# Performance work log

Hardware: AMD Instinct MI355X
Metric: run time of the kernel (lower is better)

Reference implementation:

```python
import jax, jax.numpy as jnp
import numpy as np


def _conv3x3(x, W, b):
    # NCHW conv, stride 1, padding 1 (hard-coded in the torch module)
    y = jax.lax.conv_general_dilated(
        x, W, window_strides=(1, 1), padding=[(1, 1), (1, 1)],
        dimension_numbers=("NCHW", "OIHW", "NCHW"))
    return y + b[None, :, None, None]


def _grid_sample_bilinear(img, gx, gy):
    # img: [N,H,W]; gx,gy: [N,H,W] normalized coords in [-1,1].
    # Matches torch grid_sample(mode='bilinear', padding_mode='zeros',
    # align_corners=False).
    N, H, W = img.shape
    ix = ((gx + 1.0) * W - 1.0) * 0.5  # unnormalized x coord
    iy = ((gy + 1.0) * H - 1.0) * 0.5  # unnormalized y coord

    x0f = jnp.floor(ix)
    y0f = jnp.floor(iy)
    x0 = x0f.astype(jnp.int32)
    y0 = y0f.astype(jnp.int32)
    x1 = x0 + 1
    y1 = y0 + 1

    # bilinear weights
    wx1 = ix - x0f
    wy1 = iy - y0f
    wx0 = 1.0 - wx1
    wy0 = 1.0 - wy1

    n_idx = jnp.arange(N)[:, None, None]

    def gather(yi, xi):
        valid = (yi >= 0) & (yi < H) & (xi >= 0) & (xi < W)
        yc = jnp.clip(yi, 0, H - 1)
        xc = jnp.clip(xi, 0, W - 1)
        v = img[n_idx, yc, xc]
        return jnp.where(valid, v, 0.0)

    return (gather(y0, x0) * (wy0 * wx0)
            + gather(y0, x1) * (wy0 * wx1)
            + gather(y1, x0) * (wy1 * wx0)
            + gather(y1, x1) * (wy1 * wx1))


def setup_inputs() -> dict:
    key = jax.random.key(0)
    ks = jax.random.split(key, 7)
    B, Cin, Cout, H, W = 16, 64, 64, 128, 128
    fan_in = Cin * 3 * 3
    std = 1.0 / np.sqrt(fan_in)
    x = jax.random.normal(ks[0], (B, Cin, H, W), dtype=jnp.float32)
    Ws = jax.random.normal(ks[1], (Cout, Cin, 3, 3), dtype=jnp.float32) * std
    Wx = jax.random.normal(ks[2], (Cout, Cin, 3, 3), dtype=jnp.float32) * std
    Wy = jax.random.normal(ks[3], (Cout, Cin, 3, 3), dtype=jnp.float32) * std
    bs = jnp.zeros((Cout,), dtype=jnp.float32)
    bx = jnp.zeros((Cout,), dtype=jnp.float32)
    by = jnp.zeros((Cout,), dtype=jnp.float32)
    return {"x": x, "Ws": Ws, "bs": bs, "Wx": Wx, "bx": bx, "Wy": Wy, "by": by}


def reference(x, Ws, bs, Wx, bx, Wy, by):
    score = _conv3x3(x, Ws, bs)            # [B,C,H,W]
    gx = _conv3x3(x, Wx, bx)               # absolute grid x coords
    gy = _conv3x3(x, Wy, by)               # absolute grid y coords
    B, C, H, W = score.shape
    out = _grid_sample_bilinear(score.reshape(B * C, H, W),
                                gx.reshape(B * C, H, W),
                                gy.reshape(B * C, H, W))
    return out.reshape(B, C, H, W)
```

## Files before the change

kernel.cpp:

```cpp
#include <hip/hip_runtime.h>
#include <stdint.h>

typedef unsigned short ushort_t;
typedef _Float16 f16x8 __attribute__((ext_vector_type(8)));
typedef _Float16 f16x4 __attribute__((ext_vector_type(4)));
typedef float f32x4 __attribute__((ext_vector_type(4)));
typedef float f32x16 __attribute__((ext_vector_type(16)));
typedef int   i32x4 __attribute__((ext_vector_type(4)));
typedef int   i32x16 __attribute__((ext_vector_type(16)));
typedef unsigned int uint4v __attribute__((ext_vector_type(4)));

#define HW_ 16384
#define MFMAH  __builtin_amdgcn_mfma_f32_32x32x16_f16
#define MFMAI8 __builtin_amdgcn_mfma_i32_32x32x32_i8
#define C_CORR (1.0f/16777216.0f)

__device__ __forceinline__ ushort_t f2h_bits(float f){
  union { _Float16 h; ushort_t u; } c; c.h = (_Float16)f; return c.u;
}
__device__ __forceinline__ float h_bits2f(ushort_t u){
  union { _Float16 h; ushort_t u; } c; c.u = u; return (float)c.h;
}
__device__ __forceinline__ int clamp8(int v){ return min(max(v,-127),127); }

__global__ __launch_bounds__(256) void k_repack(
    const float* __restrict__ Ws, const float* __restrict__ Wx,
    const float* __restrict__ Wy,
    ushort_t* __restrict__ WpH, unsigned int* __restrict__ WpC){
  int e = blockIdx.x*256 + threadIdx.x;
  if (e < 110592){
    int j = e & 7; int lane = (e >> 3) & 63; int rest = e >> 9;
    int ks = rest % 36; int cm = rest / 36;
    int conv = cm >> 1; int mh = cm & 1;
    int co = mh*32 + (lane & 31);
    int tap = ks >> 2;
    int ci = (ks & 3)*16 + ((lane >> 5) & 1)*8 + j;
    const float* src = (conv==0) ? Ws : (conv==1) ? Wx : Wy;
    WpH[e] = f2h_bits(src[(co*64 + ci)*9 + tap]);
  } else if (e < 110592 + 36864){
    int d = e - 110592;
    int j4 = d & 3; int lane = (d >> 2) & 63; int rest = d >> 8;
    int ks = rest % 18; int gm = rest / 18;
    int g = gm >> 1; int mh = gm & 1;
    int co = mh*32 + (lane & 31);
    int tap = ks >> 1;
    const float* src = (g==0 || g==2) ? Wx : Wy;
    unsigned dd = 0;
    #pragma unroll
    for (int bb=0; bb<4; bb++){
      int ci = (ks & 1)*32 + ((lane >> 5) & 1)*16 + j4*4 + bb;
      float w = src[(co*64 + ci)*9 + tap];
      int v;
      if (g < 2){
        v = clamp8((int)rintf(w*512.f));
      } else {
        float wl = w - h_bits2f(f2h_bits(w));
        v = clamp8((int)rintf(wl*1048576.f));
      }
      dd |= ((unsigned)(v & 255)) << (bb*8);
    }
    WpC[d] = dd;
  }
}

__global__ __launch_bounds__(512, 2) void k_conv_all(
    const float* __restrict__ x,
    const ushort_t* __restrict__ WpH, const unsigned int* __restrict__ WpC,
    const float* __restrict__ bs, const float* __restrict__ bx,
    const float* __restrict__ by,
    ushort_t* __restrict__ score, unsigned int* __restrict__ coords){
  int bid = blockIdx.x;
  int idx = bid >> 3;
  int b = (bid & 7) + 8*(idx >> 6);
  int rest = idx & 63;
  int h0 = (rest >> 2)*8;
  int wq = (rest & 3)*32;
  int t = threadIdx.x; int lane = t & 63; int wid = t >> 6;
  int n = lane & 31; int kh = lane >> 5;
  __shared__ __align__(16) _Float16 BH[10*34*64];
  __shared__ __align__(16) char BAl[10*34*64];
  __shared__ __align__(16) char BAh[10*34*64];

  const float* xb = x + (size_t)b*64*HW_;
  #pragma unroll
  for (int it=0; it<3; it++){
    int f = it*512 + t;
    if (f < 1360){
      int r = f/136; int rem = f - r*136; int q = rem/34; int w1 = rem - q*34;
      int y = h0 + r - 1; int w = wq + w1 - 1;
      f16x8 h0v = {0,0,0,0,0,0,0,0}, h1v = {0,0,0,0,0,0,0,0};
      unsigned alb[4] = {0,0,0,0}, ahb[4] = {0,0,0,0};
      if (((unsigned)y < 128u) & ((unsigned)w < 128u)){
        const float* p = xb + (size_t)(q*16)*HW_ + y*128 + w;
        #pragma unroll
        for (int j=0; j<16; j++){
          float v = p[(size_t)j*HW_];
          _Float16 hv = (_Float16)v;
          float al = v - (float)hv;
          int a8 = clamp8((int)rintf(al*32768.f));
          int x8 = clamp8((int)rintf(v*16.f));
          if (j < 8) h0v[j] = hv; else h1v[j-8] = hv;
          alb[j>>2] |= ((unsigned)(a8 & 255)) << ((j&3)*8);
          ahb[j>>2] |= ((unsigned)(x8 & 255)) << ((j&3)*8);
        }
      }
      int base = (r*34 + w1)*64;
      int sw = w1 & 7;
      *(f16x8*)&BH[base + (((2*q)   ^ sw) << 3)] = h0v;
      *(f16x8*)&BH[base + (((2*q+1) ^ sw) << 3)] = h1v;
      int islot = ((q + (w1 >> 1)) & 3) << 4;
      i32x4 av  = {(int)alb[0],(int)alb[1],(int)alb[2],(int)alb[3]};
      i32x4 hv2 = {(int)ahb[0],(int)ahb[1],(int)ahb[2],(int)ahb[3]};
      *(i32x4*)&BAl[base + islot] = av;
      *(i32x4*)&BAh[base + islot] = hv2;
    }
  }
  __syncthreads();

  int mh = wid & 1;
  int pp = wid >> 1;

  f32x16 acc_s0, acc_gx0, acc_gy0, acc_s1, acc_gx1, acc_gy1;
  i32x16 c_x0, c_y0, c_x1, c_y1;
  #pragma unroll
  for (int r2=0; r2<16; r2++){
    acc_s0[r2]=0.f; acc_gx0[r2]=0.f; acc_gy0[r2]=0.f;
    acc_s1[r2]=0.f; acc_gx1[r2]=0.f; acc_gy1[r2]=0.f;
    c_x0[r2]=0; c_y0[r2]=0; c_x1[r2]=0; c_y1[r2]=0;
  }

  const ushort_t* pS = WpH + ((0*2+mh)*36)*512 + lane*8;
  const ushort_t* pX = WpH + ((1*2+mh)*36)*512 + lane*8;
  const ushort_t* pY = WpH + ((2*2+mh)*36)*512 + lane*8;
  const char* pWhx = (const char*)WpC + (((0*2+mh)*18)*64 + lane)*16;
  const char* pWhy = (const char*)WpC + (((1*2+mh)*18)*64 + lane)*16;
  const char* pWlx = (const char*)WpC + (((2*2+mh)*18)*64 + lane)*16;
  const char* pWly = (const char*)WpC + (((3*2+mh)*18)*64 + lane)*16;

  #define ROWBLK(ROWB, AS_, AX_, AY_, CX_, CY_) do {                    \
    f16x8 bA  = *(const f16x8*)&BH[(ROWB) + off0];                      \
    f16x8 bB  = *(const f16x8*)&BH[(ROWB) + off1];                      \
    i32x4 bal = *(const i32x4*)&BAl[(ROWB) + islot];                    \
    i32x4 bah = *(const i32x4*)&BAh[(ROWB) + islot];                    \
    AS_ = MFMAH(sA, bA, AS_, 0,0,0);                                    \
    AX_ = MFMAH(xA, bA, AX_, 0,0,0);                                    \
    AY_ = MFMAH(yA, bA, AY_, 0,0,0);                                    \
    AS_ = MFMAH(sB, bB, AS_, 0,0,0);                                    \
    AX_ = MFMAH(xB, bB, AX_, 0,0,0);                                    \
    AY_ = MFMAH(yB, bB, AY_, 0,0,0);                                    \
    CX_ = MFMAI8(whx, bal, CX_, 0,0,0);                                 \
    CX_ = MFMAI8(wlx, bah, CX_, 0,0,0);                                 \
    CY_ = MFMAI8(why, bal, CY_, 0,0,0);                                 \
    CY_ = MFMAI8(wly, bah, CY_, 0,0,0);                                 \
  } while(0)

  #pragma unroll 1
  for (int ks=0; ks<18; ++ks){
    int tap = ks >> 1; int qp = ks & 1;
    int rb = tap/3; int dw = tap - rb*3 - 1;
    int w1 = n + dw + 1;
    int sw = w1 & 7;
    int rowb0 = ((rb + 2*pp)*34 + w1)*64;
    int rowb1 = rowb0 + 34*64;
    int off0  = ((qp*4 + kh)     ^ sw) << 3;
    int off1  = ((qp*4 + 2 + kh) ^ sw) << 3;
    int islot = (((qp*2 + kh) + (w1 >> 1)) & 3) << 4;
    f16x8 sA = *(const f16x8*)pS;
    f16x8 sB = *(const f16x8*)(pS + 512);
    f16x8 xA = *(const f16x8*)pX;
    f16x8 xB = *(const f16x8*)(pX + 512);
    f16x8 yA = *(const f16x8*)pY;
    f16x8 yB = *(const f16x8*)(pY + 512);
    i32x4 whx = *(const i32x4*)pWhx;
    i32x4 why = *(const i32x4*)pWhy;
    i32x4 wlx = *(const i32x4*)pWlx;
    i32x4 wly = *(const i32x4*)pWly;
    ROWBLK(rowb0, acc_s0, acc_gx0, acc_gy0, c_x0, c_y0);
    ROWBLK(rowb1, acc_s1, acc_gx1, acc_gy1, c_x1, c_y1);
    pS += 1024; pX += 1024; pY += 1024;
    pWhx += 1024; pWhy += 1024; pWlx += 1024; pWly += 1024;
  }
  #undef ROWBLK

  int w = wq + n;
  int hb = h0 + 2*pp;
  #define EPILOG(AS_, AX_, AY_, CX_, CY_, H_) do {                      \
    ushort_t*     sb = score  + (size_t)b*64*HW_ + (H_)*128 + w;        \
    unsigned int* cb = coords + (size_t)b*64*HW_ + (H_)*128 + w;        \
    _Pragma("unroll")                                                   \
    for (int reg=0; reg<16; reg++){                                     \
      int col = mh*32 + (reg & 3) + 8*(reg >> 2) + 4*kh;                \
      float sv = AS_[reg] + bs[col];                                    \
      float gx = AX_[reg] + (float)CX_[reg]*C_CORR + bx[col];           \
      float gy = AY_[reg] + (float)CY_[reg]*C_CORR + by[col];           \
      __builtin_nontemporal_store(f2h_bits(sv), &sb[(size_t)col*HW_]);  \
      float ixf = fminf(fmaxf((gx + 1.f)*64.f - 0.5f, -2.f), 129.f);    \
      float iyf = fminf(fmaxf((gy + 1.f)*64.f - 0.5f, -2.f), 129.f);    \
      unsigned ux = (unsigned)rintf((ixf + 4.f)*480.f);                 \
      unsigned uy = (unsigned)rintf((iyf + 4.f)*480.f);                 \
      __builtin_nontemporal_store(ux | (uy << 16), &cb[(size_t)col*HW_]); \
    }                                                                   \
  } while(0)
  EPILOG(acc_s0, acc_gx0, acc_gy0, c_x0, c_y0, hb);
  EPILOG(acc_s1, acc_gx1, acc_gy1, c_x1, c_y1, hb+1);
  #undef EPILOG
}

__global__ __launch_bounds__(256, 4) void k_sample(
    const ushort_t* __restrict__ score, const unsigned int* __restrict__ coords,
    float* __restrict__ out){
  int bid = blockIdx.x;
  int idx = bid >> 3;
  int b  = (bid & 7) + 8*(idx >> 6);
  int co = idx & 63;
  int t = threadIdx.x;
  __shared__ __align__(16) unsigned int SC32[135*68];

  #pragma unroll
  for (int i=0;i<9;i++){
    int c = i*256 + t;
    if (c < 2295){
      uint4v z = {0,0,0,0};
      *(uint4v*)&SC32[c*4] = z;
    }
  }
  __syncthreads();

  const ushort_t* sp = score + (size_t)(b*64 + co)*HW_;
  ushort_t* scu = (ushort_t*)SC32;
  #pragma unroll
  for (int i=0;i<8;i++){
    int c = i*256 + t;
    int y = c >> 4; int xg = (c & 15)*8;
    f16x8 v = __builtin_nontemporal_load((const f16x8*)(sp + c*8));
    f16x4 lo = {v[0],v[1],v[2],v[3]};
    f16x4 hi = {v[4],v[5],v[6],v[7]};
    *(f16x4*)&scu[(y+4)*136 + (xg+4)] = lo;
    *(f16x4*)&scu[(y+4)*136 + (xg+8)] = hi;
  }
  __syncthreads();

  const unsigned int* cp = coords + (size_t)(b*64 + co)*HW_;
  float* op = out + (size_t)(b*64 + co)*HW_;
  uint4v ca  = __builtin_nontemporal_load((const uint4v*)(cp + t*8));
  uint4v cb2 = __builtin_nontemporal_load((const uint4v*)(cp + t*8 + 4));
  #pragma unroll 1
  for (int k=0;k<8;k++){
    int px = (k*256 + t)*8;
    uint4v na, nb;
    if (k < 7){
      na = __builtin_nontemporal_load((const uint4v*)(cp + px + 2048));
      nb = __builtin_nontemporal_load((const uint4v*)(cp + px + 2052));
    }
    float r[8];
    #pragma unroll
    for (int j=0;j<8;j++){
      unsigned u = (j < 4) ? ca[j] : cb2[j-4];
      float ixp = (float)(u & 0xffffu)*(1.0f/480.0f);
      float iyp = (float)(u >> 16)   *(1.0f/480.0f);
      float x0f = floorf(ixp), y0f = floorf(iyp);
      int x0 = (int)x0f, y0 = (int)y0f;
      float wx1 = ixp - x0f, wy1 = iyp - y0f;
      float wx0 = 1.f - wx1, wy0 = 1.f - wy1;
      int base = y0*68 + (x0 >> 1);
      unsigned d00 = SC32[base],    d01 = SC32[base+1];
      unsigned d10 = SC32[base+68], d11 = SC32[base+69];
      unsigned sh = (unsigned)(x0 & 1) << 4;
      unsigned p0 = (unsigned)(((((unsigned long long)d01) << 32) | d00) >> sh);
      unsigned p1 = (unsigned)(((((unsigned long long)d11) << 32) | d10) >> sh);
      float v00 = h_bits2f((ushort_t)(p0 & 0xffffu));
      float v01 = h_bits2f((ushort_t)(p0 >> 16));
      float v10 = h_bits2f((ushort_t)(p1 & 0xffffu));
      float v11 = h_bits2f((ushort_t)(p1 >> 16));
      r[j] = wy0*(v00*wx0 + v01*wx1) + wy1*(v10*wx0 + v11*wx1);
    }
    f32x4 r0 = {r[0],r[1],r[2],r[3]};
    f32x4 r1 = {r[4],r[5],r[6],r[7]};
    __builtin_nontemporal_store(r0, (f32x4*)(op + px));
    __builtin_nontemporal_store(r1, (f32x4*)(op + px + 4));
    ca = na; cb2 = nb;
  }
}

extern "C" void kernel_launch(void* const* d_in, const int* in_sizes, int n_in,
                              void* d_out, int out_size, void* d_ws, size_t ws_size,
                              hipStream_t stream){
  const float* x  = (const float*)d_in[0];
  const float* Ws = (const float*)d_in[1];
  const float* bs = (const float*)d_in[2];
  const float* Wx = (const float*)d_in[3];
  const float* bx = (const float*)d_in[4];
  const float* Wy = (const float*)d_in[5];
  const float* by = (const float*)d_in[6];
  float* out = (float*)d_out;
  ushort_t* ws  = (ushort_t*)d_ws;
  ushort_t*     score  = ws;
  unsigned int* coords = (unsigned int*)(ws + 16777216);
  ushort_t*     WpH    = ws + 50331648;
  unsigned int* WpC    = (unsigned int*)(ws + 50331648 + 110592);

  k_repack  <<<dim3(576),  256, 0, stream>>>(Ws, Wx, Wy, WpH, WpC);
  k_conv_all<<<dim3(1024), 512, 0, stream>>>(x, WpH, WpC, bs, bx, by, score, coords);
  k_sample  <<<dim3(1024), 256, 0, stream>>>(score, coords, out);
}
```

Before: 265.1 us.

## Stage conv weights into double-buffered LDS via global_load_lds prefetch

Per-wave global loads of the packed fp16 and int8 weight fragments are replaced by a cooperative, double-buffered LDS staging scheme. Each k-step's weights are fetched with global_load_lds one step ahead, and all waves read them from shared memory. This removes redundant global and L2 weight traffic from the four waves sharing each half, and hides load latency behind the MFMAs. In exchange it adds a vmcnt wait and a block-wide barrier every iteration and uses 40KB more LDS, which may cut occupancy below the two blocks per CU the launch bounds request.

```diff
diff --git a/kernel.cpp b/kernel.cpp
--- a/kernel.cpp
+++ b/kernel.cpp
@@ -22,6 +22,12 @@
   union { _Float16 h; ushort_t u; } c; c.u = u; return (float)c.h;
 }
 __device__ __forceinline__ int clamp8(int v){ return min(max(v,-127),127); }
+
+__device__ __forceinline__ void gload_lds16(const void* g, void* l){
+  __builtin_amdgcn_global_load_lds(
+      (const __attribute__((address_space(1))) unsigned int*)g,
+      (__attribute__((address_space(3))) unsigned int*)l, 16, 0, 0);
+}
 
 __global__ __launch_bounds__(256) void k_repack(
     const float* __restrict__ Ws, const float* __restrict__ Wx,
@@ -80,6 +86,22 @@
   __shared__ __align__(16) _Float16 BH[10*34*64];
   __shared__ __align__(16) char BAl[10*34*64];
   __shared__ __align__(16) char BAh[10*34*64];
+  __shared__ __align__(16) char WL[2][20][1024];
+
+  #define STAGE_W(KS, BB) do {                                           \
+    for (int c = wid; c < 20; c += 8){                                   \
+      int mh2 = (c >= 10) ? 1 : 0; int frag = c - mh2*10;                \
+      const char* srcp;                                                  \
+      if (frag < 6){ int cv = frag >> 1; int hf = frag & 1;              \
+        srcp = (const char*)WpH + ((cv*2+mh2)*36 + 2*(KS) + hf)*1024;    \
+      } else { int g = frag - 6;                                         \
+        srcp = (const char*)WpC + ((g*2+mh2)*18 + (KS))*1024;            \
+      }                                                                  \
+      gload_lds16(srcp + (size_t)lane*16, &WL[BB][c][0]);                \
+    }                                                                    \
+  } while(0)
+
+  STAGE_W(0, 0);
 
   const float* xb = x + (size_t)b*64*HW_;
   #pragma unroll
@@ -115,6 +137,7 @@
       *(i32x4*)&BAh[base + islot] = hv2;
     }
   }
+  asm volatile("s_waitcnt vmcnt(0)" ::: "memory");
   __syncthreads();
 
   int mh = wid & 1;
@@ -129,13 +152,7 @@
     c_x0[r2]=0; c_y0[r2]=0; c_x1[r2]=0; c_y1[r2]=0;
   }
 
-  const ushort_t* pS = WpH + ((0*2+mh)*36)*512 + lane*8;
-  const ushort_t* pX = WpH + ((1*2+mh)*36)*512 + lane*8;
-  const ushort_t* pY = WpH + ((2*2+mh)*36)*512 + lane*8;
-  const char* pWhx = (const char*)WpC + (((0*2+mh)*18)*64 + lane)*16;
-  const char* pWhy = (const char*)WpC + (((1*2+mh)*18)*64 + lane)*16;
-  const char* pWlx = (const char*)WpC + (((2*2+mh)*18)*64 + lane)*16;
-  const char* pWly = (const char*)WpC + (((3*2+mh)*18)*64 + lane)*16;
+  int wbase = mh*10;
 
   #define ROWBLK(ROWB, AS_, AX_, AY_, CX_, CY_) do {                    \
     f16x8 bA  = *(const f16x8*)&BH[(ROWB) + off0];                      \
@@ -154,8 +171,10 @@
     CY_ = MFMAI8(wly, bah, CY_, 0,0,0);                                 \
   } while(0)
 
+  int buf = 0;
   #pragma unroll 1
   for (int ks=0; ks<18; ++ks){
+    if (ks < 17) STAGE_W(ks+1, buf^1);
     int tap = ks >> 1; int qp = ks & 1;
     int rb = tap/3; int dw = tap - rb*3 - 1;
     int w1 = n + dw + 1;
@@ -165,22 +184,25 @@
     int off0  = ((qp*4 + kh)     ^ sw) << 3;
     int off1  = ((qp*4 + 2 + kh) ^ sw) << 3;
     int islot = (((qp*2 + kh) + (w1 >> 1)) & 3) << 4;
-    f16x8 sA = *(const f16x8*)pS;
-    f16x8 sB = *(const f16x8*)(pS + 512);
-    f16x8 xA = *(const f16x8*)pX;
-    f16x8 xB = *(const f16x8*)(pX + 512);
-    f16x8 yA = *(const f16x8*)pY;
-    f16x8 yB = *(const f16x8*)(pY + 512);
-    i32x4 whx = *(const i32x4*)pWhx;
-    i32x4 why = *(const i32x4*)pWhy;
-    i32x4 wlx = *(const i32x4*)pWlx;
-    i32x4 wly = *(const i32x4*)pWly;
+    const char* wb = &WL[buf][wbase][0];
+    f16x8 sA = *(const f16x8*)(wb + 0*1024 + lane*16);
+    f16x8 sB = *(const f16x8*)(wb + 1*1024 + lane*16);
+    f16x8 xA = *(const f16x8*)(wb + 2*1024 + lane*16);
+    f16x8 xB = *(const f16x8*)(wb + 3*1024 + lane*16);
+    f16x8 yA = *(const f16x8*)(wb + 4*1024 + lane*16);
+    f16x8 yB = *(const f16x8*)(wb + 5*1024 + lane*16);
+    i32x4 whx = *(const i32x4*)(wb + 6*1024 + lane*16);
+    i32x4 why = *(const i32x4*)(wb + 7*1024 + lane*16);
+    i32x4 wlx = *(const i32x4*)(wb + 8*1024 + lane*16);
+    i32x4 wly = *(const i32x4*)(wb + 9*1024 + lane*16);
     ROWBLK(rowb0, acc_s0, acc_gx0, acc_gy0, c_x0, c_y0);
     ROWBLK(rowb1, acc_s1, acc_gx1, acc_gy1, c_x1, c_y1);
-    pS += 1024; pX += 1024; pY += 1024;
-    pWhx += 1024; pWhy += 1024; pWlx += 1024; pWly += 1024;
+    asm volatile("s_waitcnt vmcnt(0)" ::: "memory");
+    __syncthreads();
+    buf ^= 1;
   }
   #undef ROWBLK
+  #undef STAGE_W
 
   int w = wq + n;
   int hb = h0 + 2*pp;
```

New measurement: 268.6 us. No clear change (+1.3%).
